# Optimization experiments

Measured on AMD Instinct MI355X. Metric: run time of the kernel, lower is better.

Reference implementation:

```python
import jax, jax.numpy as jnp
import numpy as np

INPUT_DIM = 512
OUTPUT_DIM = 128
MAX_DEPTH = 5          # internal nodes at depths 0..4, leaves at depth 5
BATCH = 16384
N_INT = 2**MAX_DEPTH - 1        # 31 internal nodes (heap order: node i children 2i+1, 2i+2)
N_ALL = 2**(MAX_DEPTH + 1) - 1  # 63 nodes total, each owns a leaf vector


def setup_inputs() -> dict:
    key = jax.random.key(0)
    k0, k1, k2, k3, k4 = jax.random.split(key, 5)
    x = jax.random.normal(k0, (BATCH, INPUT_DIM), dtype=jnp.float32)
    lim = 1.0 / np.sqrt(INPUT_DIM)  # torch nn.Linear default init range
    W = jax.random.uniform(k1, (N_INT, 2, INPUT_DIM), jnp.float32, -lim, lim)
    b = jax.random.uniform(k2, (N_INT, 2), jnp.float32, -lim, lim)
    # gamma initialized to [0.5, 0.5] in the module; perturb slightly so it's not degenerate
    gamma = 0.5 + 0.02 * jax.random.normal(k3, (N_INT, 2), dtype=jnp.float32)
    leaf = jax.random.normal(k4, (N_ALL, OUTPUT_DIM), dtype=jnp.float32)
    return {"x": x, "W": W, "b": b, "gamma": gamma, "leaf": leaf}


def reference(x, W, b, gamma, leaf):
    """Level-by-level (bottom-up) vectorized evaluation of the recursive MixNode tree.

    Per internal node n (heap-indexed):
      router = softmax(x @ W[n].T + b[n])                      # soft routing path of route()
      children = left * router[:,0] + right * router[:,1]      # stack + bmm
      g = softmax(gamma[n])
      y = g[0] * children + g[1] * leaf[n]                     # stack + matmul(gamma)
    Pure leaves (depth == max_depth) return leaf broadcast over batch.
    """
    B = x.shape[0]
    # depth-5 pure leaves: heap indices 31..62 -> Y: [B, 32, O]
    Y = jnp.broadcast_to(leaf[N_INT:N_ALL][None], (B, 2**MAX_DEPTH, leaf.shape[-1]))
    for d in range(MAX_DEPTH - 1, -1, -1):
        s, e = 2**d - 1, 2**(d + 1) - 1   # internal nodes at depth d
        logits = jnp.einsum('bi,nji->bnj', x, W[s:e]) + b[s:e]   # [B, 2^d, 2]
        r = jax.nn.softmax(logits, axis=-1)
        left, right = Y[:, 0::2], Y[:, 1::2]                      # children in heap order
        comb = left * r[..., 0:1] + right * r[..., 1:2]           # [B, 2^d, O]
        g = jax.nn.softmax(gamma[s:e], axis=-1)                   # [2^d, 2]
        Y = g[None, :, 0:1] * comb + g[None, :, 1:2] * leaf[s:e][None]
    return Y[:, 0]  # root output [B, O]
```

## Files before the change

### kernel.cpp

```cpp
#include <hip/hip_runtime.h>
#include <hip/hip_bf16.h>
#include <cstdint>

#define BATCH   16384
#define INDIM   512
#define OUTDIM  128
#define NINT    31
#define BM      64
#define THREADS 256

#define WS_WBF    0u
#define WS_LEAFT  65536u
#define WS_BIAS   81920u
#define WS_GSM0   82176u
#define WS_GSM1   82432u

typedef __attribute__((ext_vector_type(8))) short s8v;
typedef __attribute__((ext_vector_type(4))) float f4v;

__device__ __forceinline__ short bfs(float f) {
    return (short)__builtin_bit_cast(unsigned short, __float2bfloat16(f));
}
__device__ __forceinline__ unsigned int pk2(float lo, float hi) {
    return (unsigned int)(unsigned short)bfs(lo) |
           ((unsigned int)(unsigned short)bfs(hi) << 16);
}

#define SWZ(r, k) ((k) ^ (((r) & 7) << 3))

__global__ __launch_bounds__(256) void prep_kernel(
    const float* __restrict__ W, const float* __restrict__ bvec,
    const float* __restrict__ gamma, const float* __restrict__ leaf,
    unsigned char* __restrict__ ws)
{
    unsigned short* wbf = (unsigned short*)(ws + WS_WBF);
    unsigned short* lT  = (unsigned short*)(ws + WS_LEAFT);
    float* bias = (float*)(ws + WS_BIAS);
    float* g0v  = (float*)(ws + WS_GSM0);
    float* g1v  = (float*)(ws + WS_GSM1);
    const int tid  = blockIdx.x * 256 + threadIdx.x;
    const int nthr = gridDim.x * 256;

    for (int i = tid; i < 64 * INDIM; i += nthr) {
        int r = i >> 9;
        float v = (r < 62) ? W[i] : 0.0f;
        wbf[i] = (unsigned short)bfs(v);
    }
    for (int i = tid; i < OUTDIM * 64; i += nthr) {
        int n = i & 63, col = i >> 6;
        float v = (n < 63) ? leaf[(size_t)n * OUTDIM + col] : 0.0f;
        lT[i] = (unsigned short)bfs(v);
    }
    if (tid < 64) bias[tid] = (tid < 62) ? bvec[tid] : 0.0f;
    if (tid < NINT) {
        float a = gamma[2*tid], b = gamma[2*tid+1];
        float m = fmaxf(a, b);
        float e0 = __expf(a - m), e1 = __expf(b - m);
        float inv = 1.0f / (e0 + e1);
        g0v[tid] = e0 * inv;
        g1v[tid] = e1 * inv;
    }
}

__global__ __launch_bounds__(THREADS) void mix_main(
    const float* __restrict__ x, const unsigned char* __restrict__ ws,
    float* __restrict__ out)
{
    __shared__ __align__(16) float Lg[BM][65];
    __shared__ __align__(16) unsigned short cbf[BM][64];

    const int t    = threadIdx.x;
    const int lane = t & 63;
    const int wv   = t >> 6;
    const int g    = lane >> 4;
    const int lm   = lane & 15;
    const int row0 = blockIdx.x * BM;

    const float* bias = (const float*)(ws + WS_BIAS);
    f4v acc[4];
    #pragma unroll
    for (int c = 0; c < 4; ++c) {
        float b = bias[16*c + lm];
        acc[c] = (f4v){b, b, b, b};
    }

    const float* xrow = x + (size_t)(row0 + 16*wv + lm) * INDIM;
    const unsigned short* wb = (const unsigned short*)(ws + WS_WBF);
    #pragma unroll
    for (int ks = 0; ks < INDIM / 32; ++ks) {
        const int k0 = ks * 32 + 8 * g;
        float4 x0 = *(const float4*)(xrow + k0);
        float4 x1 = *(const float4*)(xrow + k0 + 4);
        s8v a;
        a[0] = bfs(x0.x); a[1] = bfs(x0.y); a[2] = bfs(x0.z); a[3] = bfs(x0.w);
        a[4] = bfs(x1.x); a[5] = bfs(x1.y); a[6] = bfs(x1.z); a[7] = bfs(x1.w);
        #pragma unroll
        for (int c = 0; c < 4; ++c) {
            s8v b = *(const s8v*)(wb + (size_t)(16*c + lm) * INDIM + k0);
            acc[c] = __builtin_amdgcn_mfma_f32_16x16x32_bf16(a, b, acc[c], 0, 0, 0);
        }
    }
    #pragma unroll
    for (int c = 0; c < 4; ++c)
        #pragma unroll
        for (int r = 0; r < 4; ++r)
            Lg[16*wv + 4*g + r][16*c + lm] = acc[c][r];
    __syncthreads();

    if (t < BM) {
        const int row = t;
        const float* g0v = (const float*)(ws + WS_GSM0);
        const float* g1v = (const float*)(ws + WS_GSM1);
        float Pp[63];
        float cv[64];
        Pp[0] = 1.0f;
        #pragma unroll
        for (int n = 0; n < NINT; ++n) {
            float l0 = Lg[row][2*n];
            float l1 = Lg[row][2*n + 1];
            float r1 = 1.0f / (1.0f + __expf(l0 - l1));
            float base = Pp[n] * g0v[n];
            Pp[2*n + 1] = base * (1.0f - r1);
            Pp[2*n + 2] = base * r1;
            cv[n] = Pp[n] * g1v[n];
        }
        #pragma unroll
        for (int n = NINT; n < 63; ++n) cv[n] = Pp[n];
        cv[63] = 0.0f;
        #pragma unroll
        for (int c2 = 0; c2 < 8; ++c2) {
            int p = SWZ(row, 8 * c2);
            *(uint4*)&cbf[row][p] = make_uint4(
                pk2(cv[8*c2+0], cv[8*c2+1]), pk2(cv[8*c2+2], cv[8*c2+3]),
                pk2(cv[8*c2+4], cv[8*c2+5]), pk2(cv[8*c2+6], cv[8*c2+7]));
        }
    }
    __syncthreads();

    const unsigned short* lT = (const unsigned short*)(ws + WS_LEAFT);
    f4v o[8] = {};
    #pragma unroll
    for (int kw = 0; kw < 2; ++kw) {
        const int k0 = kw * 32 + 8 * g;
        s8v a = *(const s8v*)&cbf[16*wv + lm][SWZ(lm, k0)];
        #pragma unroll
        for (int nt = 0; nt < 8; ++nt) {
            s8v b = *(const s8v*)(lT + (size_t)(16*nt + lm) * 64 + k0);
            o[nt] = __builtin_amdgcn_mfma_f32_16x16x32_bf16(a, b, o[nt], 0, 0, 0);
        }
    }
    #pragma unroll
    for (int nt = 0; nt < 8; ++nt)
        #pragma unroll
        for (int r = 0; r < 4; ++r)
            out[(size_t)(row0 + 16*wv + 4*g + r) * OUTDIM + 16*nt + lm] = o[nt][r];
}

extern "C" void kernel_launch(void* const* d_in, const int* in_sizes, int n_in,
                              void* d_out, int out_size, void* d_ws, size_t ws_size,
                              hipStream_t stream) {
    const float* x     = (const float*)d_in[0];
    const float* W     = (const float*)d_in[1];
    const float* b     = (const float*)d_in[2];
    const float* gamma = (const float*)d_in[3];
    const float* leaf  = (const float*)d_in[4];
    float* out = (float*)d_out;
    hipLaunchKernelGGL(prep_kernel, dim3(64), dim3(256), 0, stream,
                       W, b, gamma, leaf, (unsigned char*)d_ws);
    hipLaunchKernelGGL(mix_main, dim3(BATCH / BM), dim3(THREADS), 0, stream,
                       x, (const unsigned char*)d_ws, out);
}
```

Before: 95.51 us.

## Split K dimension across 16 waves with LDS reduction of routing logits

Raises the block from 4 to 16 waves. Each group of 4 waves handles a quarter of the 512-wide input, and the partial logits are reduced in shared memory. The output GEMM is also split so each wave computes 2 of the 8 output column tiles, and the gamma softmax values are cached in LDS. The aim is more memory-level parallelism and latency hiding for the x stream, which the 256-thread block limited. In exchange it adds a larger LDS footprint, an extra reduction pass and barrier, and blocks of 1024 threads that may cut occupancy.

New measurement: 96.03 us. Within noise of the previous version (+0.5%).

```diff
diff --git a/kernel.cpp b/kernel.cpp
--- a/kernel.cpp
+++ b/kernel.cpp
@@ -7,7 +7,7 @@
 #define OUTDIM  128
 #define NINT    31
 #define BM      64
-#define THREADS 256
+#define THREADS 1024
 
 #define WS_WBF    0u
 #define WS_LEAFT  65536u
@@ -66,28 +66,36 @@
     const float* __restrict__ x, const unsigned char* __restrict__ ws,
     float* __restrict__ out)
 {
-    __shared__ __align__(16) float Lg[BM][65];
+    __shared__ __align__(16) float Lgp[4][BM][65];
     __shared__ __align__(16) unsigned short cbf[BM][64];
+    __shared__ float gsh0[NINT], gsh1[NINT];
 
     const int t    = threadIdx.x;
     const int lane = t & 63;
-    const int wv   = t >> 6;
+    const int w    = t >> 6;
+    const int rg   = w & 3;
+    const int kg   = w >> 2;
     const int g    = lane >> 4;
     const int lm   = lane & 15;
     const int row0 = blockIdx.x * BM;
+
+    if (t < NINT) {
+        gsh0[t] = ((const float*)(ws + WS_GSM0))[t];
+        gsh1[t] = ((const float*)(ws + WS_GSM1))[t];
+    }
 
     const float* bias = (const float*)(ws + WS_BIAS);
     f4v acc[4];
     #pragma unroll
     for (int c = 0; c < 4; ++c) {
-        float b = bias[16*c + lm];
+        float b = (kg == 0) ? bias[16*c + lm] : 0.0f;
         acc[c] = (f4v){b, b, b, b};
     }
 
-    const float* xrow = x + (size_t)(row0 + 16*wv + lm) * INDIM;
-    const unsigned short* wb = (const unsigned short*)(ws + WS_WBF);
+    const float* xrow = x + (size_t)(row0 + 16*rg + lm) * INDIM + 128*kg;
+    const unsigned short* wb = (const unsigned short*)(ws + WS_WBF) + 128*kg;
     #pragma unroll
-    for (int ks = 0; ks < INDIM / 32; ++ks) {
+    for (int ks = 0; ks < 4; ++ks) {
         const int k0 = ks * 32 + 8 * g;
         float4 x0 = *(const float4*)(xrow + k0);
         float4 x1 = *(const float4*)(xrow + k0 + 4);
@@ -104,56 +112,69 @@
     for (int c = 0; c < 4; ++c)
         #pragma unroll
         for (int r = 0; r < 4; ++r)
-            Lg[16*wv + 4*g + r][16*c + lm] = acc[c][r];
+            Lgp[kg][16*rg + 4*g + r][16*c + lm] = acc[c][r];
+    __syncthreads();
+
+    {
+        const int row = t >> 4;
+        const int c0  = (t & 15) * 4;
+        #pragma unroll
+        for (int j = 0; j < 4; ++j) {
+            const int c = c0 + j;
+            Lgp[0][row][c] += Lgp[1][row][c] + Lgp[2][row][c] + Lgp[3][row][c];
+        }
+    }
     __syncthreads();
 
     if (t < BM) {
         const int row = t;
-        const float* g0v = (const float*)(ws + WS_GSM0);
-        const float* g1v = (const float*)(ws + WS_GSM1);
         float Pp[63];
-        float cv[64];
+        unsigned int cvp[32];
+        float sv = 0.0f;
         Pp[0] = 1.0f;
         #pragma unroll
         for (int n = 0; n < NINT; ++n) {
-            float l0 = Lg[row][2*n];
-            float l1 = Lg[row][2*n + 1];
+            float l0 = Lgp[0][row][2*n];
+            float l1 = Lgp[0][row][2*n + 1];
             float r1 = 1.0f / (1.0f + __expf(l0 - l1));
-            float base = Pp[n] * g0v[n];
+            float base = Pp[n] * gsh0[n];
             Pp[2*n + 1] = base * (1.0f - r1);
             Pp[2*n + 2] = base * r1;
-            cv[n] = Pp[n] * g1v[n];
+            float cval = Pp[n] * gsh1[n];
+            if (n & 1) cvp[n >> 1] = pk2(sv, cval); else sv = cval;
         }
         #pragma unroll
-        for (int n = NINT; n < 63; ++n) cv[n] = Pp[n];
-        cv[63] = 0.0f;
+        for (int n = NINT; n < 63; ++n) {
+            float cval = Pp[n];
+            if (n & 1) cvp[n >> 1] = pk2(sv, cval); else sv = cval;
+        }
+        cvp[31] = pk2(sv, 0.0f);
         #pragma unroll
-        for (int c2 = 0; c2 < 8; ++c2) {
-            int p = SWZ(row, 8 * c2);
-            *(uint4*)&cbf[row][p] = make_uint4(
-                pk2(cv[8*c2+0], cv[8*c2+1]), pk2(cv[8*c2+2], cv[8*c2+3]),
-                pk2(cv[8*c2+4], cv[8*c2+5]), pk2(cv[8*c2+6], cv[8*c2+7]));
+        for (int j = 0; j < 8; ++j) {
+            int p = SWZ(row, 8 * j);
+            *(uint4*)&cbf[row][p] =
+                make_uint4(cvp[4*j], cvp[4*j+1], cvp[4*j+2], cvp[4*j+3]);
         }
     }
     __syncthreads();
 
     const unsigned short* lT = (const unsigned short*)(ws + WS_LEAFT);
-    f4v o[8] = {};
+    f4v o[2] = {};
     #pragma unroll
     for (int kw = 0; kw < 2; ++kw) {
         const int k0 = kw * 32 + 8 * g;
-        s8v a = *(const s8v*)&cbf[16*wv + lm][SWZ(lm, k0)];
+        s8v a = *(const s8v*)&cbf[16*rg + lm][SWZ(lm, k0)];
         #pragma unroll
-        for (int nt = 0; nt < 8; ++nt) {
-            s8v b = *(const s8v*)(lT + (size_t)(16*nt + lm) * 64 + k0);
-            o[nt] = __builtin_amdgcn_mfma_f32_16x16x32_bf16(a, b, o[nt], 0, 0, 0);
+        for (int j = 0; j < 2; ++j) {
+            s8v b = *(const s8v*)(lT + (size_t)(16*(2*kg + j) + lm) * 64 + k0);
+            o[j] = __builtin_amdgcn_mfma_f32_16x16x32_bf16(a, b, o[j], 0, 0, 0);
         }
     }
     #pragma unroll
-    for (int nt = 0; nt < 8; ++nt)
+    for (int j = 0; j < 2; ++j)
         #pragma unroll
         for (int r = 0; r < 4; ++r)
-            out[(size_t)(row0 + 16*wv + 4*g + r) * OUTDIM + 16*nt + lm] = o[nt][r];
+            out[(size_t)(row0 + 16*rg + 4*g + r) * OUTDIM + 16*(2*kg + j) + lm] = o[j][r];
 }
 
 extern "C" void kernel_launch(void* const* d_in, const int* in_sizes, int n_in,
@@ -165,7 +186,7 @@
     const float* gamma = (const float*)d_in[3];
     const float* leaf  = (const float*)d_in[4];
     float* out = (float*)d_out;
-    hipLaunchKernelGGL(prep_kernel, dim3(64), dim3(256), 0, stream,
+    hipLaunchKernelGGL(prep_kernel, dim3(128), dim3(256), 0, stream,
                        W, b, gamma, leaf, (unsigned char*)d_ws);
     hipLaunchKernelGGL(mix_main, dim3(BATCH / BM), dim3(THREADS), 0, stream,
                        x, (const unsigned char*)d_ws, out);
```
